# Performance work log

Hardware: AMD Instinct MI355X
Metric: run time of the kernel (lower is better)

## Reference

```python
import jax, jax.numpy as jnp
import numpy as np

NUM_AGENTS = 8
OBSERVATION_SIZE = 30
INPUT_SHAPE = 4 + 2 * OBSERVATION_SIZE  # 64
STATE_SHAPE = INPUT_SHAPE * NUM_AGENTS  # 512
HYPER_HIDDEN_DIM = 40
QMIX_HIDDEN_DIM = 40


def setup_inputs() -> dict:
    key = jax.random.key(0)
    ks = jax.random.split(key, 16)
    E, T = 256, 256

    def lin(k, fan_in, fan_out):
        kw, kb = jax.random.split(k)
        bound = 1.0 / np.sqrt(fan_in)
        w = jax.random.uniform(kw, (fan_in, fan_out), jnp.float32, -bound, bound)
        b = jax.random.uniform(kb, (fan_out,), jnp.float32, -bound, bound)
        return w, b

    hw1_w0, hw1_b0 = lin(ks[0], STATE_SHAPE, HYPER_HIDDEN_DIM)
    hw1_w1, hw1_b1 = lin(ks[1], HYPER_HIDDEN_DIM, NUM_AGENTS * QMIX_HIDDEN_DIM)
    hw2_w0, hw2_b0 = lin(ks[2], STATE_SHAPE, HYPER_HIDDEN_DIM)
    hw2_w1, hw2_b1 = lin(ks[3], HYPER_HIDDEN_DIM, QMIX_HIDDEN_DIM)
    hb1_w, hb1_b = lin(ks[4], STATE_SHAPE, QMIX_HIDDEN_DIM)
    hb2_w0, hb2_b0 = lin(ks[5], STATE_SHAPE, QMIX_HIDDEN_DIM)
    hb2_w1, hb2_b1 = lin(ks[6], QMIX_HIDDEN_DIM, 1)

    return {
        "q_values": jax.random.normal(ks[7], (E, T, NUM_AGENTS), jnp.float32),
        "states": jax.random.normal(ks[8], (E, T, STATE_SHAPE), jnp.float32),
        "hw1_w0": hw1_w0, "hw1_b0": hw1_b0, "hw1_w1": hw1_w1, "hw1_b1": hw1_b1,
        "hw2_w0": hw2_w0, "hw2_b0": hw2_b0, "hw2_w1": hw2_w1, "hw2_b1": hw2_b1,
        "hb1_w": hb1_w, "hb1_b": hb1_b,
        "hb2_w0": hb2_w0, "hb2_b0": hb2_b0, "hb2_w1": hb2_w1, "hb2_b1": hb2_b1,
    }


def reference(q_values, states, hw1_w0, hw1_b0, hw1_w1, hw1_b1,
              hw2_w0, hw2_b0, hw2_w1, hw2_b1,
              hb1_w, hb1_b, hb2_w0, hb2_b0, hb2_w1, hb2_b1):
    E = q_values.shape[0]
    q = q_values.reshape(-1, NUM_AGENTS)          # [B, A]
    s = states.reshape(-1, STATE_SHAPE)           # [B, S]

    # hyper_w1: Linear-ReLU-Linear -> abs -> [B, A, H]
    w1 = jnp.abs(jax.nn.relu(s @ hw1_w0 + hw1_b0) @ hw1_w1 + hw1_b1)
    w1 = w1.reshape(-1, NUM_AGENTS, QMIX_HIDDEN_DIM)
    b1 = s @ hb1_w + hb1_b                        # [B, H]

    hidden = jax.nn.elu(jnp.einsum('ba,bah->bh', q, w1) + b1)  # [B, H]

    # hyper_w2 -> abs -> [B, H]; hyper_b2 -> [B, 1]
    w2 = jnp.abs(jax.nn.relu(s @ hw2_w0 + hw2_b0) @ hw2_w1 + hw2_b1)
    b2 = jax.nn.relu(s @ hb2_w0 + hb2_b0) @ hb2_w1 + hb2_b1    # [B, 1]

    q_total = jnp.einsum('bh,bh->b', hidden, w2)[:, None] + b2  # [B, 1]
    return q_total.reshape(E, -1, 1)
```

## Files before the change

### kernel.cpp

```cpp
#include <hip/hip_runtime.h>
#include <math.h>

#define NA 8
#define SS 512
#define BROWS 32
#define NTHREADS 320

typedef __attribute__((ext_vector_type(8))) short bf16x8;
typedef __attribute__((ext_vector_type(4))) float f32x4;
typedef __attribute__((ext_vector_type(4))) unsigned u32x4;

static __device__ __forceinline__ unsigned short f2bf(float f) {
    union { float f; unsigned u; } v; v.f = f;
    unsigned r = v.u + 0x7FFFu + ((v.u >> 16) & 1u);
    return (unsigned short)(r >> 16);
}
static __device__ __forceinline__ float bf2f(unsigned short u) {
    union { unsigned u; float f; } v; v.u = ((unsigned)u) << 16; return v.f;
}
static __device__ __forceinline__ unsigned pk2(float lo, float hi) {
    return (unsigned)f2bf(lo) | ((unsigned)f2bf(hi) << 16);
}
static __device__ __forceinline__ bf16x8 cvt8(float4 a, float4 b) {
    u32x4 t;
    t[0] = pk2(a.x, a.y);
    t[1] = pk2(a.z, a.w);
    t[2] = pk2(b.x, b.y);
    t[3] = pk2(b.z, b.w);
    return __builtin_bit_cast(bf16x8, t);
}

#define BP_OFF   0
#define BP1_OFF  81920
#define BP2_OFF  102400
#define BIAS0_BYTE 210944

__global__ void prep_kernel(const float* __restrict__ hw1_w0, const float* __restrict__ hb1_w,
                            const float* __restrict__ hw2_w0, const float* __restrict__ hb2_w0,
                            const float* __restrict__ hw1_w1, const float* __restrict__ hw2_w1,
                            const float* __restrict__ hw1_b0, const float* __restrict__ hb1_b,
                            const float* __restrict__ hw2_b0, const float* __restrict__ hb2_b0,
                            unsigned short* __restrict__ ws16, float* __restrict__ bias0) {
    int idx = blockIdx.x * blockDim.x + threadIdx.x;
    if (idx < 81920) {
        int i = idx & 7, l = (idx >> 3) & 63, t = idx >> 9;
        int kt = t & 15, nt = t >> 4;
        int k = kt * 32 + (l >> 4) * 8 + i;
        int n = nt * 16 + (l & 15);
        int seg = n / 40, c = n - seg * 40;
        const float* src = (seg == 0) ? hw1_w0 : (seg == 1) ? hb1_w : (seg == 2) ? hw2_w0 : hb2_w0;
        ws16[BP_OFF + idx] = f2bf(src[k * 40 + c]);
    } else if (idx < 81920 + 20480) {
        int j = idx - 81920;
        int i = j & 7, l = (j >> 3) & 63, t = j >> 9;
        int kt = t & 1, nt = t >> 1;
        int k = kt * 32 + (l >> 4) * 8 + i;
        int n = nt * 16 + (l & 15);
        float v = (k < 40) ? hw1_w1[k * 320 + n] : 0.f;
        ws16[BP1_OFF + j] = f2bf(v);
    } else if (idx < 81920 + 20480 + 3072) {
        int j = idx - 102400;
        int i = j & 7, l = (j >> 3) & 63, t = j >> 9;
        int kt = t & 1, nt = t >> 1;
        int k = kt * 32 + (l >> 4) * 8 + i;
        int n = nt * 16 + (l & 15);
        float v = (k < 40 && n < 40) ? hw2_w1[k * 40 + n] : 0.f;
        ws16[BP2_OFF + j] = f2bf(v);
    } else if (idx < 81920 + 20480 + 3072 + 160) {
        int j = idx - 105472;
        int seg = j / 40, c = j - seg * 40;
        const float* b = (seg == 0) ? hw1_b0 : (seg == 1) ? hb1_b : (seg == 2) ? hw2_b0 : hb2_b0;
        bias0[j] = b[c];
    }
}

#define W1_STRIDE 324
#define W1_OFF    0
#define B1_OFF    20736
#define H1_OFF    26496
#define H2_OFF    30592
#define W2_OFF    34688
#define B2_OFF    37248
#define SMEM_BYTES 37504

__global__ __launch_bounds__(NTHREADS, 4) void qmix_kernel(
    const float* __restrict__ q_values, const float* __restrict__ states,
    const unsigned short* __restrict__ Bp, const unsigned short* __restrict__ Bp1,
    const unsigned short* __restrict__ Bp2, const float* __restrict__ bias0,
    const float* __restrict__ hw1_b1, const float* __restrict__ hw2_b1,
    const float* __restrict__ hb2_w1, const float* __restrict__ hb2_b1,
    float* __restrict__ out)
{
    __shared__ __align__(16) char smem[SMEM_BYTES];
    const int tid = threadIdx.x;
    const int wv = tid >> 6;
    const int l = tid & 63;
    const int p = l & 15;
    const int row0 = blockIdx.x * BROWS;

    const int rq = tid & 31;
    const float4* qp = (const float4*)(q_values + (size_t)(row0 + rq) * NA);
    float4 qa = qp[0], qb = qp[1];

    const int c0 = wv * 32 + p, c1 = c0 + 16;
    const float bia0v = bias0[c0], bia1v = bias0[c1];
    const float hbw0 = (c0 >= 120) ? hb2_w1[c0 - 120] : 0.f;
    const float hbw1 = (c1 >= 120) ? hb2_w1[c1 - 120] : 0.f;
    float hb1v[4];
    #pragma unroll
    for (int t = 0; t < 4; ++t) hb1v[t] = hw1_b1[(wv * 4 + t) * 16 + p];
    const int n2 = wv * 16 + p;
    const float hb2v = (n2 < 40) ? hw2_b1[n2] : 0.f;
    const float hb2b = hb2_b1[0];

    for (int idx = tid; idx < 32 * 24; idx += NTHREADS) {
        int r = idx / 24, k = 40 + (idx - r * 24);
        int byte = (r * 128 + k * 2) ^ ((r & 7) << 4);
        *(unsigned short*)(smem + H1_OFF + byte) = 0;
        *(unsigned short*)(smem + H2_OFF + byte) = 0;
    }

    f32x4 acc[2][2] = {};
    {
        const float* Arow0 = states + (size_t)(row0 + p) * SS + (l >> 4) * 8;
        const float* Arow1 = Arow0 + 16 * SS;
        const unsigned short* bp0 = Bp + (size_t)((wv * 2 + 0) * 16) * 512 + (size_t)l * 8;
        const unsigned short* bp1 = Bp + (size_t)((wv * 2 + 1) * 16) * 512 + (size_t)l * 8;
        #pragma unroll
        for (int kt = 0; kt < 16; ++kt) {
            float4 x0 = *(const float4*)(Arow0 + kt * 32);
            float4 x1 = *(const float4*)(Arow0 + kt * 32 + 4);
            float4 y0 = *(const float4*)(Arow1 + kt * 32);
            float4 y1 = *(const float4*)(Arow1 + kt * 32 + 4);
            bf16x8 b0 = *(const bf16x8*)(bp0 + kt * 512);
            bf16x8 b1 = *(const bf16x8*)(bp1 + kt * 512);
            bf16x8 a0 = cvt8(x0, x1);
            bf16x8 a1 = cvt8(y0, y1);
            acc[0][0] = __builtin_amdgcn_mfma_f32_16x16x32_bf16(a0, b0, acc[0][0], 0, 0, 0);
            acc[0][1] = __builtin_amdgcn_mfma_f32_16x16x32_bf16(a0, b1, acc[0][1], 0, 0, 0);
            acc[1][0] = __builtin_amdgcn_mfma_f32_16x16x32_bf16(a1, b0, acc[1][0], 0, 0, 0);
            acc[1][1] = __builtin_amdgcn_mfma_f32_16x16x32_bf16(a1, b1, acc[1][1], 0, 0, 0);
        }
    }

    {
        float rs[2][4] = {{0.f,0.f,0.f,0.f},{0.f,0.f,0.f,0.f}};
        float* b1buf = (float*)(smem + B1_OFF);
        #pragma unroll
        for (int ntl = 0; ntl < 2; ++ntl) {
            const int c = wv * 32 + ntl * 16 + p;
            const float bia = ntl ? bia1v : bia0v;
            const float hbw = ntl ? hbw1 : hbw0;
            #pragma unroll
            for (int mt = 0; mt < 2; ++mt)
            #pragma unroll
            for (int g = 0; g < 4; ++g) {
                const int row = mt * 16 + (l >> 4) * 4 + g;
                const float v = acc[mt][ntl][g] + bia;
                if (c < 40) {
                    *(unsigned short*)(smem + H1_OFF + ((row * 128 + c * 2) ^ ((row & 7) << 4)))
                        = f2bf(fmaxf(v, 0.f));
                } else if (c < 80) {
                    b1buf[row * 45 + (c - 40)] = v;
                } else if (c < 120) {
                    *(unsigned short*)(smem + H2_OFF + ((row * 128 + (c - 80) * 2) ^ ((row & 7) << 4)))
                        = f2bf(fmaxf(v, 0.f));
                } else {
                    rs[mt][g] += fmaxf(v, 0.f) * hbw;
                }
            }
        }
        if (wv >= 3) {
            float* B2 = (float*)(smem + B2_OFF);
            #pragma unroll
            for (int mt = 0; mt < 2; ++mt)
            #pragma unroll
            for (int g = 0; g < 4; ++g) {
                float r2 = rs[mt][g];
                r2 += __shfl_xor(r2, 1);
                r2 += __shfl_xor(r2, 2);
                r2 += __shfl_xor(r2, 4);
                r2 += __shfl_xor(r2, 8);
                if (p == 0) B2[(wv - 3) * 32 + mt * 16 + (l >> 4) * 4 + g] = r2;
            }
        }
    }
    __syncthreads();

    {
        char* H1 = smem + H1_OFF;
        const int kch = (l >> 4) * 16;
        f32x4 wacc[2][4] = {};
        #pragma unroll
        for (int kt = 0; kt < 2; ++kt) {
            bf16x8 a[2];
            #pragma unroll
            for (int mt = 0; mt < 2; ++mt) {
                int row = mt * 16 + p;
                a[mt] = *(const bf16x8*)(H1 + ((row * 128 + kt * 64 + kch) ^ ((row & 7) << 4)));
            }
            #pragma unroll
            for (int t = 0; t < 4; ++t) {
                int nt1 = wv * 4 + t;
                bf16x8 b = *(const bf16x8*)(Bp1 + ((size_t)(nt1 * 2 + kt) * 64 + l) * 8);
                wacc[0][t] = __builtin_amdgcn_mfma_f32_16x16x32_bf16(a[0], b, wacc[0][t], 0, 0, 0);
                wacc[1][t] = __builtin_amdgcn_mfma_f32_16x16x32_bf16(a[1], b, wacc[1][t], 0, 0, 0);
            }
        }
        unsigned short* W1 = (unsigned short*)(smem + W1_OFF);
        #pragma unroll
        for (int mt = 0; mt < 2; ++mt)
        #pragma unroll
        for (int t = 0; t < 4; ++t)
        #pragma unroll
        for (int g = 0; g < 4; ++g) {
            int row = mt * 16 + (l >> 4) * 4 + g;
            int n = (wv * 4 + t) * 16 + p;
            W1[row * W1_STRIDE + n] = f2bf(fabsf(wacc[mt][t][g] + hb1v[t]));
        }
        if (wv < 3) {
            char* H2 = smem + H2_OFF;
            f32x4 c2[2] = {};
            #pragma unroll
            for (int kt = 0; kt < 2; ++kt) {
                bf16x8 a[2];
                #pragma unroll
                for (int mt = 0; mt < 2; ++mt) {
                    int row = mt * 16 + p;
                    a[mt] = *(const bf16x8*)(H2 + ((row * 128 + kt * 64 + kch) ^ ((row & 7) << 4)));
                }
                bf16x8 b = *(const bf16x8*)(Bp2 + ((size_t)(wv * 2 + kt) * 64 + l) * 8);
                c2[0] = __builtin_amdgcn_mfma_f32_16x16x32_bf16(a[0], b, c2[0], 0, 0, 0);
                c2[1] = __builtin_amdgcn_mfma_f32_16x16x32_bf16(a[1], b, c2[1], 0, 0, 0);
            }
            unsigned short* W2 = (unsigned short*)(smem + W2_OFF);
            #pragma unroll
            for (int mt = 0; mt < 2; ++mt)
            #pragma unroll
            for (int g = 0; g < 4; ++g) {
                int row = mt * 16 + (l >> 4) * 4 + g;
                int n = wv * 16 + p;
                if (n < 40) W2[row * 40 + n] = f2bf(fabsf(c2[mt][g] + hb2v));
            }
        }
    }
    __syncthreads();

    {
        float* b1buf = (float*)(smem + B1_OFF);
        unsigned short* W1 = (unsigned short*)(smem + W1_OFF);
        unsigned short* W2 = (unsigned short*)(smem + W2_OFF);
        float* PR = (float*)(smem + H1_OFF);
        const int r = tid & 31;
        const int gq = tid >> 5;
        float qv[8] = {qa.x, qa.y, qa.z, qa.w, qb.x, qb.y, qb.z, qb.w};
        float psum = 0.f;
        #pragma unroll
        for (int kk = 0; kk < 4; ++kk) {
            int h = gq * 4 + kk;
            float acc2 = b1buf[r * 45 + h];
            #pragma unroll
            for (int a = 0; a < 8; ++a) acc2 += qv[a] * bf2f(W1[r * W1_STRIDE + a * 40 + h]);
            float hid = (acc2 > 0.f) ? acc2 : expm1f(acc2);
            psum += hid * bf2f(W2[r * 40 + h]);
        }
        PR[tid] = psum;
    }
    __syncthreads();
    if (tid < 32) {
        float* PR = (float*)(smem + H1_OFF);
        float* B2 = (float*)(smem + B2_OFF);
        float s = B2[tid] + B2[32 + tid] + hb2b;
        #pragma unroll
        for (int g = 0; g < 10; ++g) s += PR[g * 32 + tid];
        out[row0 + tid] = s;
    }
}

extern "C" void kernel_launch(void* const* d_in, const int* in_sizes, int n_in,
                              void* d_out, int out_size, void* d_ws, size_t ws_size,
                              hipStream_t stream) {
    const float* q_values = (const float*)d_in[0];
    const float* states   = (const float*)d_in[1];
    const float* hw1_w0 = (const float*)d_in[2];
    const float* hw1_b0 = (const float*)d_in[3];
    const float* hw1_w1 = (const float*)d_in[4];
    const float* hw1_b1 = (const float*)d_in[5];
    const float* hw2_w0 = (const float*)d_in[6];
    const float* hw2_b0 = (const float*)d_in[7];
    const float* hw2_w1 = (const float*)d_in[8];
    const float* hw2_b1 = (const float*)d_in[9];
    const float* hb1_w  = (const float*)d_in[10];
    const float* hb1_b  = (const float*)d_in[11];
    const float* hb2_w0 = (const float*)d_in[12];
    const float* hb2_b0 = (const float*)d_in[13];
    const float* hb2_w1 = (const float*)d_in[14];
    const float* hb2_b1 = (const float*)d_in[15];

    unsigned short* ws16 = (unsigned short*)d_ws;
    float* bias0 = (float*)((char*)d_ws + BIAS0_BYTE);

    const int prep_total = 81920 + 20480 + 3072 + 160;
    prep_kernel<<<(prep_total + 255) / 256, 256, 0, stream>>>(
        hw1_w0, hb1_w, hw2_w0, hb2_w0, hw1_w1, hw2_w1,
        hw1_b0, hb1_b, hw2_b0, hb2_b0, ws16, bias0);

    const int B = in_sizes[0] / NA;
    qmix_kernel<<<B / BROWS, NTHREADS, 0, stream>>>(
        q_values, states,
        ws16 + BP_OFF, ws16 + BP1_OFF, ws16 + BP2_OFF, bias0,
        hw1_b1, hw2_b1, hb2_w1, hb2_b1, (float*)d_out);
}
```

Before: 294.7 us.

## Stage states tiles through LDS with register prefetch across multiple tiles per block

Each block now processes four 32-row tiles in a loop. The next tile's states are prefetched into registers with coalesced float4 loads while the current tile runs, then converted to bf16 and written into a swizzled LDS buffer that the first MFMA reads from. Previously each lane loaded states directly from global memory in the MFMA fragment layout. The change aims to overlap the dominant HBM read of states with compute and to make those loads coalesced. In exchange it raises register use (13 float4 staging registers, launch bounds cut to 2 waves per SIMD), grows LDS use, and adds barriers per tile.

Result: slower. 400.0 us (+35.8%).

```diff
diff --git a/kernel.cpp b/kernel.cpp
--- a/kernel.cpp
+++ b/kernel.cpp
@@ -4,11 +4,11 @@
 #define NA 8
 #define SS 512
 #define BROWS 32
+#define TPB 4
 #define NTHREADS 320
 
 typedef __attribute__((ext_vector_type(8))) short bf16x8;
 typedef __attribute__((ext_vector_type(4))) float f32x4;
-typedef __attribute__((ext_vector_type(4))) unsigned u32x4;
 
 static __device__ __forceinline__ unsigned short f2bf(float f) {
     union { float f; unsigned u; } v; v.f = f;
@@ -17,17 +17,6 @@
 }
 static __device__ __forceinline__ float bf2f(unsigned short u) {
     union { unsigned u; float f; } v; v.u = ((unsigned)u) << 16; return v.f;
-}
-static __device__ __forceinline__ unsigned pk2(float lo, float hi) {
-    return (unsigned)f2bf(lo) | ((unsigned)f2bf(hi) << 16);
-}
-static __device__ __forceinline__ bf16x8 cvt8(float4 a, float4 b) {
-    u32x4 t;
-    t[0] = pk2(a.x, a.y);
-    t[1] = pk2(a.z, a.w);
-    t[2] = pk2(b.x, b.y);
-    t[3] = pk2(b.z, b.w);
-    return __builtin_bit_cast(bf16x8, t);
 }
 
 #define BP_OFF   0
@@ -76,14 +65,15 @@
 
 #define W1_STRIDE 324
 #define W1_OFF    0
-#define B1_OFF    20736
-#define H1_OFF    26496
-#define H2_OFF    30592
-#define W2_OFF    34688
-#define B2_OFF    37248
-#define SMEM_BYTES 37504
-
-__global__ __launch_bounds__(NTHREADS, 4) void qmix_kernel(
+#define PR_OFF    24576
+#define B1_OFF    32768
+#define H1_OFF    38528
+#define H2_OFF    42624
+#define W2_OFF    46720
+#define B2_OFF    49280
+#define SMEM_BYTES 49536
+
+__global__ __launch_bounds__(NTHREADS, 2) void qmix_kernel(
     const float* __restrict__ q_values, const float* __restrict__ states,
     const unsigned short* __restrict__ Bp, const unsigned short* __restrict__ Bp1,
     const unsigned short* __restrict__ Bp2, const float* __restrict__ bias0,
@@ -96,11 +86,7 @@
     const int wv = tid >> 6;
     const int l = tid & 63;
     const int p = l & 15;
-    const int row0 = blockIdx.x * BROWS;
-
-    const int rq = tid & 31;
-    const float4* qp = (const float4*)(q_values + (size_t)(row0 + rq) * NA);
-    float4 qa = qp[0], qb = qp[1];
+    const int blkrow0 = blockIdx.x * (BROWS * TPB);
 
     const int c0 = wv * 32 + p, c1 = c0 + 16;
     const float bia0v = bias0[c0], bia1v = bias0[c1];
@@ -120,160 +106,195 @@
         *(unsigned short*)(smem + H2_OFF + byte) = 0;
     }
 
-    f32x4 acc[2][2] = {};
-    {
-        const float* Arow0 = states + (size_t)(row0 + p) * SS + (l >> 4) * 8;
-        const float* Arow1 = Arow0 + 16 * SS;
-        const unsigned short* bp0 = Bp + (size_t)((wv * 2 + 0) * 16) * 512 + (size_t)l * 8;
-        const unsigned short* bp1 = Bp + (size_t)((wv * 2 + 1) * 16) * 512 + (size_t)l * 8;
+    const float4* sg = (const float4*)(states + (size_t)blkrow0 * SS);
+    float4 stg[13];
+    #pragma unroll
+    for (int i = 0; i < 13; ++i) {
+        int idx = i * NTHREADS + tid;
+        if (idx < BROWS * (SS / 4)) stg[i] = sg[idx];
+    }
+
+    for (int t = 0; t < TPB; ++t) {
+        const int row0 = blkrow0 + t * BROWS;
+        __syncthreads();
+
         #pragma unroll
-        for (int kt = 0; kt < 16; ++kt) {
-            float4 x0 = *(const float4*)(Arow0 + kt * 32);
-            float4 x1 = *(const float4*)(Arow0 + kt * 32 + 4);
-            float4 y0 = *(const float4*)(Arow1 + kt * 32);
-            float4 y1 = *(const float4*)(Arow1 + kt * 32 + 4);
-            bf16x8 b0 = *(const bf16x8*)(bp0 + kt * 512);
-            bf16x8 b1 = *(const bf16x8*)(bp1 + kt * 512);
-            bf16x8 a0 = cvt8(x0, x1);
-            bf16x8 a1 = cvt8(y0, y1);
-            acc[0][0] = __builtin_amdgcn_mfma_f32_16x16x32_bf16(a0, b0, acc[0][0], 0, 0, 0);
-            acc[0][1] = __builtin_amdgcn_mfma_f32_16x16x32_bf16(a0, b1, acc[0][1], 0, 0, 0);
-            acc[1][0] = __builtin_amdgcn_mfma_f32_16x16x32_bf16(a1, b0, acc[1][0], 0, 0, 0);
-            acc[1][1] = __builtin_amdgcn_mfma_f32_16x16x32_bf16(a1, b1, acc[1][1], 0, 0, 0);
-        }
-    }
-
-    {
-        float rs[2][4] = {{0.f,0.f,0.f,0.f},{0.f,0.f,0.f,0.f}};
-        float* b1buf = (float*)(smem + B1_OFF);
-        #pragma unroll
-        for (int ntl = 0; ntl < 2; ++ntl) {
-            const int c = wv * 32 + ntl * 16 + p;
-            const float bia = ntl ? bia1v : bia0v;
-            const float hbw = ntl ? hbw1 : hbw0;
-            #pragma unroll
-            for (int mt = 0; mt < 2; ++mt)
-            #pragma unroll
-            for (int g = 0; g < 4; ++g) {
-                const int row = mt * 16 + (l >> 4) * 4 + g;
-                const float v = acc[mt][ntl][g] + bia;
-                if (c < 40) {
-                    *(unsigned short*)(smem + H1_OFF + ((row * 128 + c * 2) ^ ((row & 7) << 4)))
-                        = f2bf(fmaxf(v, 0.f));
-                } else if (c < 80) {
-                    b1buf[row * 45 + (c - 40)] = v;
-                } else if (c < 120) {
-                    *(unsigned short*)(smem + H2_OFF + ((row * 128 + (c - 80) * 2) ^ ((row & 7) << 4)))
-                        = f2bf(fmaxf(v, 0.f));
-                } else {
-                    rs[mt][g] += fmaxf(v, 0.f) * hbw;
-                }
-            }
-        }
-        if (wv >= 3) {
-            float* B2 = (float*)(smem + B2_OFF);
-            #pragma unroll
-            for (int mt = 0; mt < 2; ++mt)
-            #pragma unroll
-            for (int g = 0; g < 4; ++g) {
-                float r2 = rs[mt][g];
-                r2 += __shfl_xor(r2, 1);
-                r2 += __shfl_xor(r2, 2);
-                r2 += __shfl_xor(r2, 4);
-                r2 += __shfl_xor(r2, 8);
-                if (p == 0) B2[(wv - 3) * 32 + mt * 16 + (l >> 4) * 4 + g] = r2;
-            }
-        }
-    }
-    __syncthreads();
-
-    {
-        char* H1 = smem + H1_OFF;
-        const int kch = (l >> 4) * 16;
-        f32x4 wacc[2][4] = {};
-        #pragma unroll
-        for (int kt = 0; kt < 2; ++kt) {
-            bf16x8 a[2];
-            #pragma unroll
-            for (int mt = 0; mt < 2; ++mt) {
-                int row = mt * 16 + p;
-                a[mt] = *(const bf16x8*)(H1 + ((row * 128 + kt * 64 + kch) ^ ((row & 7) << 4)));
-            }
-            #pragma unroll
-            for (int t = 0; t < 4; ++t) {
-                int nt1 = wv * 4 + t;
-                bf16x8 b = *(const bf16x8*)(Bp1 + ((size_t)(nt1 * 2 + kt) * 64 + l) * 8);
-                wacc[0][t] = __builtin_amdgcn_mfma_f32_16x16x32_bf16(a[0], b, wacc[0][t], 0, 0, 0);
-                wacc[1][t] = __builtin_amdgcn_mfma_f32_16x16x32_bf16(a[1], b, wacc[1][t], 0, 0, 0);
-            }
-        }
-        unsigned short* W1 = (unsigned short*)(smem + W1_OFF);
-        #pragma unroll
-        for (int mt = 0; mt < 2; ++mt)
-        #pragma unroll
-        for (int t = 0; t < 4; ++t)
-        #pragma unroll
-        for (int g = 0; g < 4; ++g) {
-            int row = mt * 16 + (l >> 4) * 4 + g;
-            int n = (wv * 4 + t) * 16 + p;
-            W1[row * W1_STRIDE + n] = f2bf(fabsf(wacc[mt][t][g] + hb1v[t]));
-        }
-        if (wv < 3) {
-            char* H2 = smem + H2_OFF;
-            f32x4 c2[2] = {};
+        for (int i = 0; i < 13; ++i) {
+            int idx = i * NTHREADS + tid;
+            if (idx < BROWS * (SS / 4)) {
+                int r = idx >> 7, c4 = idx & 127;
+                float4 v = stg[i];
+                ushort4 b;
+                b.x = f2bf(v.x); b.y = f2bf(v.y); b.z = f2bf(v.z); b.w = f2bf(v.w);
+                int byte = (r * 1024 + c4 * 8) ^ ((r & 7) << 4);
+                *(ushort4*)(smem + byte) = b;
+            }
+        }
+        if (t + 1 < TPB) {
+            const float4* sgn = sg + (size_t)(t + 1) * (BROWS * (SS / 4));
+            #pragma unroll
+            for (int i = 0; i < 13; ++i) {
+                int idx = i * NTHREADS + tid;
+                if (idx < BROWS * (SS / 4)) stg[i] = sgn[idx];
+            }
+        }
+        const float4* qp = (const float4*)(q_values + (size_t)(row0 + (tid & 31)) * NA);
+        float4 qa = qp[0], qb = qp[1];
+        __syncthreads();
+
+        f32x4 acc[2][2] = {};
+        {
+            const int kch = (l >> 4) * 16;
+            const int r0 = p;
+            const int r1 = r0 + 16;
+            const int swz0 = (r0 & 7) << 4;
+            const unsigned short* bp0 = Bp + (size_t)((wv * 2 + 0) * 16) * 512 + (size_t)l * 8;
+            const unsigned short* bp1 = Bp + (size_t)((wv * 2 + 1) * 16) * 512 + (size_t)l * 8;
+            #pragma unroll
+            for (int kt = 0; kt < 16; ++kt) {
+                bf16x8 a0 = *(const bf16x8*)(smem + ((r0 * 1024 + kt * 64 + kch) ^ swz0));
+                bf16x8 a1 = *(const bf16x8*)(smem + ((r1 * 1024 + kt * 64 + kch) ^ swz0));
+                bf16x8 b0 = *(const bf16x8*)(bp0 + kt * 512);
+                bf16x8 b1 = *(const bf16x8*)(bp1 + kt * 512);
+                acc[0][0] = __builtin_amdgcn_mfma_f32_16x16x32_bf16(a0, b0, acc[0][0], 0, 0, 0);
+                acc[0][1] = __builtin_amdgcn_mfma_f32_16x16x32_bf16(a0, b1, acc[0][1], 0, 0, 0);
+                acc[1][0] = __builtin_amdgcn_mfma_f32_16x16x32_bf16(a1, b0, acc[1][0], 0, 0, 0);
+                acc[1][1] = __builtin_amdgcn_mfma_f32_16x16x32_bf16(a1, b1, acc[1][1], 0, 0, 0);
+            }
+        }
+
+        {
+            float rs[2][4] = {{0.f,0.f,0.f,0.f},{0.f,0.f,0.f,0.f}};
+            float* b1buf = (float*)(smem + B1_OFF);
+            #pragma unroll
+            for (int ntl = 0; ntl < 2; ++ntl) {
+                const int c = wv * 32 + ntl * 16 + p;
+                const float bia = ntl ? bia1v : bia0v;
+                const float hbw = ntl ? hbw1 : hbw0;
+                #pragma unroll
+                for (int mt = 0; mt < 2; ++mt)
+                #pragma unroll
+                for (int g = 0; g < 4; ++g) {
+                    const int row = mt * 16 + (l >> 4) * 4 + g;
+                    const float v = acc[mt][ntl][g] + bia;
+                    if (c < 40) {
+                        *(unsigned short*)(smem + H1_OFF + ((row * 128 + c * 2) ^ ((row & 7) << 4)))
+                            = f2bf(fmaxf(v, 0.f));
+                    } else if (c < 80) {
+                        b1buf[row * 45 + (c - 40)] = v;
+                    } else if (c < 120) {
+                        *(unsigned short*)(smem + H2_OFF + ((row * 128 + (c - 80) * 2) ^ ((row & 7) << 4)))
+                            = f2bf(fmaxf(v, 0.f));
+                    } else {
+                        rs[mt][g] += fmaxf(v, 0.f) * hbw;
+                    }
+                }
+            }
+            if (wv >= 3) {
+                float* B2 = (float*)(smem + B2_OFF);
+                #pragma unroll
+                for (int mt = 0; mt < 2; ++mt)
+                #pragma unroll
+                for (int g = 0; g < 4; ++g) {
+                    float r2 = rs[mt][g];
+                    r2 += __shfl_xor(r2, 1);
+                    r2 += __shfl_xor(r2, 2);
+                    r2 += __shfl_xor(r2, 4);
+                    r2 += __shfl_xor(r2, 8);
+                    if (p == 0) B2[(wv - 3) * 32 + mt * 16 + (l >> 4) * 4 + g] = r2;
+                }
+            }
+        }
+        __syncthreads();
+
+        {
+            char* H1 = smem + H1_OFF;
+            const int kch = (l >> 4) * 16;
+            f32x4 wacc[2][4] = {};
             #pragma unroll
             for (int kt = 0; kt < 2; ++kt) {
                 bf16x8 a[2];
                 #pragma unroll
                 for (int mt = 0; mt < 2; ++mt) {
                     int row = mt * 16 + p;
-                    a[mt] = *(const bf16x8*)(H2 + ((row * 128 + kt * 64 + kch) ^ ((row & 7) << 4)));
-                }
-                bf16x8 b = *(const bf16x8*)(Bp2 + ((size_t)(wv * 2 + kt) * 64 + l) * 8);
-                c2[0] = __builtin_amdgcn_mfma_f32_16x16x32_bf16(a[0], b, c2[0], 0, 0, 0);
-                c2[1] = __builtin_amdgcn_mfma_f32_16x16x32_bf16(a[1], b, c2[1], 0, 0, 0);
-            }
-            unsigned short* W2 = (unsigned short*)(smem + W2_OFF);
+                    a[mt] = *(const bf16x8*)(H1 + ((row * 128 + kt * 64 + kch) ^ ((row & 7) << 4)));
+                }
+                #pragma unroll
+                for (int tt = 0; tt < 4; ++tt) {
+                    int nt1 = wv * 4 + tt;
+                    bf16x8 b = *(const bf16x8*)(Bp1 + ((size_t)(nt1 * 2 + kt) * 64 + l) * 8);
+                    wacc[0][tt] = __builtin_amdgcn_mfma_f32_16x16x32_bf16(a[0], b, wacc[0][tt], 0, 0, 0);
+                    wacc[1][tt] = __builtin_amdgcn_mfma_f32_16x16x32_bf16(a[1], b, wacc[1][tt], 0, 0, 0);
+                }
+            }
+            unsigned short* W1 = (unsigned short*)(smem + W1_OFF);
             #pragma unroll
             for (int mt = 0; mt < 2; ++mt)
+            #pragma unroll
+            for (int tt = 0; tt < 4; ++tt)
             #pragma unroll
             for (int g = 0; g < 4; ++g) {
                 int row = mt * 16 + (l >> 4) * 4 + g;
-                int n = wv * 16 + p;
-                if (n < 40) W2[row * 40 + n] = f2bf(fabsf(c2[mt][g] + hb2v));
-            }
-        }
-    }
-    __syncthreads();
-
-    {
-        float* b1buf = (float*)(smem + B1_OFF);
-        unsigned short* W1 = (unsigned short*)(smem + W1_OFF);
-        unsigned short* W2 = (unsigned short*)(smem + W2_OFF);
-        float* PR = (float*)(smem + H1_OFF);
-        const int r = tid & 31;
-        const int gq = tid >> 5;
-        float qv[8] = {qa.x, qa.y, qa.z, qa.w, qb.x, qb.y, qb.z, qb.w};
-        float psum = 0.f;
-        #pragma unroll
-        for (int kk = 0; kk < 4; ++kk) {
-            int h = gq * 4 + kk;
-            float acc2 = b1buf[r * 45 + h];
-            #pragma unroll
-            for (int a = 0; a < 8; ++a) acc2 += qv[a] * bf2f(W1[r * W1_STRIDE + a * 40 + h]);
-            float hid = (acc2 > 0.f) ? acc2 : expm1f(acc2);
-            psum += hid * bf2f(W2[r * 40 + h]);
-        }
-        PR[tid] = psum;
-    }
-    __syncthreads();
-    if (tid < 32) {
-        float* PR = (float*)(smem + H1_OFF);
-        float* B2 = (float*)(smem + B2_OFF);
-        float s = B2[tid] + B2[32 + tid] + hb2b;
-        #pragma unroll
-        for (int g = 0; g < 10; ++g) s += PR[g * 32 + tid];
-        out[row0 + tid] = s;
+                int n = (wv * 4 + tt) * 16 + p;
+                W1[row * W1_STRIDE + n] = f2bf(fabsf(wacc[mt][tt][g] + hb1v[tt]));
+            }
+            if (wv < 3) {
+                char* H2 = smem + H2_OFF;
+                f32x4 c2[2] = {};
+                #pragma unroll
+                for (int kt = 0; kt < 2; ++kt) {
+                    bf16x8 a[2];
+                    #pragma unroll
+                    for (int mt = 0; mt < 2; ++mt) {
+                        int row = mt * 16 + p;
+                        a[mt] = *(const bf16x8*)(H2 + ((row * 128 + kt * 64 + kch) ^ ((row & 7) << 4)));
+                    }
+                    bf16x8 b = *(const bf16x8*)(Bp2 + ((size_t)(wv * 2 + kt) * 64 + l) * 8);
+                    c2[0] = __builtin_amdgcn_mfma_f32_16x16x32_bf16(a[0], b, c2[0], 0, 0, 0);
+                    c2[1] = __builtin_amdgcn_mfma_f32_16x16x32_bf16(a[1], b, c2[1], 0, 0, 0);
+                }
+                unsigned short* W2 = (unsigned short*)(smem + W2_OFF);
+                #pragma unroll
+                for (int mt = 0; mt < 2; ++mt)
+                #pragma unroll
+                for (int g = 0; g < 4; ++g) {
+                    int row = mt * 16 + (l >> 4) * 4 + g;
+                    int n = wv * 16 + p;
+                    if (n < 40) W2[row * 40 + n] = f2bf(fabsf(c2[mt][g] + hb2v));
+                }
+            }
+        }
+        __syncthreads();
+
+        {
+            float* b1buf = (float*)(smem + B1_OFF);
+            unsigned short* W1 = (unsigned short*)(smem + W1_OFF);
+            unsigned short* W2 = (unsigned short*)(smem + W2_OFF);
+            float* PR = (float*)(smem + PR_OFF);
+            const int r = tid & 31;
+            const int gq = tid >> 5;
+            float qv[8] = {qa.x, qa.y, qa.z, qa.w, qb.x, qb.y, qb.z, qb.w};
+            float psum = 0.f;
+            #pragma unroll
+            for (int kk = 0; kk < 4; ++kk) {
+                int h = gq * 4 + kk;
+                float acc2 = b1buf[r * 45 + h];
+                #pragma unroll
+                for (int a = 0; a < 8; ++a) acc2 += qv[a] * bf2f(W1[r * W1_STRIDE + a * 40 + h]);
+                float hid = (acc2 > 0.f) ? acc2 : expm1f(acc2);
+                psum += hid * bf2f(W2[r * 40 + h]);
+            }
+            PR[tid] = psum;
+        }
+        __syncthreads();
+        if (tid < 32) {
+            float* PR = (float*)(smem + PR_OFF);
+            float* B2 = (float*)(smem + B2_OFF);
+            float s = B2[tid] + B2[32 + tid] + hb2b;
+            #pragma unroll
+            for (int g = 0; g < 10; ++g) s += PR[g * 32 + tid];
+            out[row0 + tid] = s;
+        }
     }
 }
 
@@ -306,7 +327,7 @@
         hw1_b0, hb1_b, hw2_b0, hb2_b0, ws16, bias0);
 
     const int B = in_sizes[0] / NA;
-    qmix_kernel<<<B / BROWS, NTHREADS, 0, stream>>>(
+    qmix_kernel<<<B / (BROWS * TPB), NTHREADS, 0, stream>>>(
         q_values, states,
         ws16 + BP_OFF, ws16 + BP1_OFF, ws16 + BP2_OFF, bias0,
         hw1_b1, hw2_b1, hb2_w1, hb2_b1, (float*)d_out);
```
